# Kernel tuning notes

Hardware: AMD Instinct MI355X
Metric: run time of the kernel (lower is better)

## Reference

```python
import jax, jax.numpy as jnp
import numpy as np

B, S, F_, D, H, L, OUT = 2, 1024, 240, 512, 6, 6, 512
NH = 16
DH = D // NH
EPS = 1e-6  # fast_transformers causal-linear eps
LN_EPS = 1e-5  # torch LayerNorm default


def layernorm(x, g, b):
    m = x.mean(-1, keepdims=True)
    v = ((x - m) ** 2).mean(-1, keepdims=True)
    return (x - m) * jax.lax.rsqrt(v + LN_EPS) * g + b


def causal_linear_attn(q, k, v):
    # q,k,v: [B,S,NH,DH]; feature map phi(x)=elu(x)+1 (fast_transformers default)
    Q = jax.nn.elu(q) + 1.0
    K = jax.nn.elu(k) + 1.0
    # running sum of outer products K_i V_i^T -> [B,S,NH,DH,DH]
    kv = jnp.cumsum(jnp.einsum('bshd,bshm->bshdm', K, v), axis=1)
    num = jnp.einsum('bshd,bshdm->bshm', Q, kv)
    Z = 1.0 / (jnp.einsum('bshd,bshd->bsh', Q, jnp.cumsum(K, axis=1)) + EPS)
    return num * Z[..., None]


def setup_inputs() -> dict:
    key = jax.random.key(0)
    ks = iter(jax.random.split(key, 16))

    def w(shape, s=0.02):
        return (s * jax.random.normal(next(ks), shape)).astype(jnp.float32)

    f32 = jnp.float32
    return {
        'x': jax.random.normal(next(ks), (B, S, F_), dtype=f32),
        'g_in': jnp.ones((F_,), f32), 'b_in': jnp.zeros((F_,), f32),
        'W_pre': w((F_, D)), 'b_pre': jnp.zeros((D,), f32),
        'Wq': w((L, D, D)), 'bq': jnp.zeros((L, D), f32),
        'Wk': w((L, D, D)), 'bk': jnp.zeros((L, D), f32),
        'Wv': w((L, D, D)), 'bv': jnp.zeros((L, D), f32),
        'Wo': w((L, D, D)), 'bo': jnp.zeros((L, D), f32),
        'W1': w((L, D, D)), 'bf1': jnp.zeros((L, D), f32),  # feed_forward_dimensions == hidden_sz
        'W2': w((L, D, D)), 'bf2': jnp.zeros((L, D), f32),
        'ln1_g': jnp.ones((L, D), f32), 'ln1_b': jnp.zeros((L, D), f32),
        'ln2_g': jnp.ones((L, D), f32), 'ln2_b': jnp.zeros((L, D), f32),
        'lnf_g': jnp.ones((D,), f32), 'lnf_b': jnp.zeros((D,), f32),
        'W_post': w((D, OUT)), 'b_post': jnp.zeros((OUT,), f32),
    }


def reference(x, g_in, b_in, W_pre, b_pre, Wq, bq, Wk, bk, Wv, bv, Wo, bo,
              W1, bf1, W2, bf2, ln1_g, ln1_b, ln2_g, ln2_b, lnf_g, lnf_b,
              W_post, b_post):
    # input norm + pre projection
    h = layernorm(x, g_in, b_in) @ W_pre + b_pre  # [B,S,D]
    # fast_transformers post-norm encoder layers
    for l in range(L):
        q = (h @ Wq[l] + bq[l]).reshape(B, S, NH, DH)
        k = (h @ Wk[l] + bk[l]).reshape(B, S, NH, DH)
        v = (h @ Wv[l] + bv[l]).reshape(B, S, NH, DH)
        a = causal_linear_attn(q, k, v).reshape(B, S, D) @ Wo[l] + bo[l]
        h = layernorm(h + a, ln1_g[l], ln1_b[l])
        y = jax.nn.relu(h @ W1[l] + bf1[l]) @ W2[l] + bf2[l]
        h = layernorm(h + y, ln2_g[l], ln2_b[l])
    # final encoder norm, then post projection
    h = layernorm(h, lnf_g, lnf_b)
    return h @ W_post + b_post
```

## Files before the change

kernel.cpp:

```cpp
#include <hip/hip_runtime.h>
#include <hip/hip_bf16.h>
#include <cmath>

#define NROW 2048
#define DMODEL 512
#define FIN 240
#define FINPAD 256
#define NHEAD 16
#define DHEAD 32
#define CHUNK 64
#define NCHUNK 16
#define NLAYER 6
#define SEQ 1024
#define QKVLD 1536

typedef __attribute__((ext_vector_type(8))) short bf16x8;
typedef __attribute__((ext_vector_type(4))) float f32x4;
typedef __attribute__((ext_vector_type(4))) unsigned short u16x4;

#define MFMA_BF16 __builtin_amdgcn_mfma_f32_16x16x32_bf16

__device__ __forceinline__ float phi(float x) {
    return x > 0.f ? x + 1.f : expf(x);
}

__device__ __forceinline__ float bf2f(unsigned short u) {
    return __uint_as_float((unsigned)u << 16);
}

__device__ __forceinline__ unsigned short f2bf_bits(float z) {
    __hip_bfloat16 hb_ = __float2bfloat16(z);
    return *reinterpret_cast<unsigned short*>(&hb_);
}

__device__ __forceinline__ void load_lds16(const void* g, void* l) {
    __builtin_amdgcn_global_load_lds(
        (const __attribute__((address_space(1))) void*)g,
        (__attribute__((address_space(3))) void*)l, 16, 0, 0);
}

__global__ __launch_bounds__(64) void ln_kernel(
    const float* __restrict__ in, const float* __restrict__ res,
    const float* __restrict__ g, const float* __restrict__ b,
    float* __restrict__ out, __hip_bfloat16* __restrict__ outb,
    int C, int Cpad) {
    int row = blockIdx.x;
    int t = threadIdx.x;
    const float* xr = in + (size_t)row * C;
    const float* rr = res ? res + (size_t)row * C : nullptr;
    f32x4 v[2] = {{0.f,0.f,0.f,0.f},{0.f,0.f,0.f,0.f}};
    float sum = 0.f, sq = 0.f;
#pragma unroll
    for (int i = 0; i < 2; ++i) {
        int c = (t + i * 64) * 4;
        if (c < C) {
            f32x4 x_ = *(const f32x4*)&xr[c];
            if (rr) x_ += *(const f32x4*)&rr[c];
            v[i] = x_;
#pragma unroll
            for (int j = 0; j < 4; ++j) { sum += x_[j]; sq += x_[j] * x_[j]; }
        }
    }
#pragma unroll
    for (int off = 32; off > 0; off >>= 1) {
        sum += __shfl_xor(sum, off, 64);
        sq  += __shfl_xor(sq,  off, 64);
    }
    float mean = sum / (float)C;
    float var  = sq / (float)C - mean * mean;
    float rstd = rsqrtf(var + 1e-5f);
#pragma unroll
    for (int i = 0; i < 2; ++i) {
        int c = (t + i * 64) * 4;
        f32x4 y;
#pragma unroll
        for (int j = 0; j < 4; ++j) y[j] = (v[i][j] - mean) * rstd;
        if (c < C) {
            f32x4 gg = *(const f32x4*)&g[c];
            f32x4 bb = *(const f32x4*)&b[c];
#pragma unroll
            for (int j = 0; j < 4; ++j) y[j] = y[j] * gg[j] + bb[j];
            if (out) *(f32x4*)&out[(size_t)row * C + c] = y;
        }
        if (outb && c < Cpad) {
            u16x4 o;
#pragma unroll
            for (int j = 0; j < 4; ++j) {
                float z = (c + j < C) ? y[j] : 0.f;
                o[j] = f2bf_bits(z);
            }
            *(u16x4*)&outb[(size_t)row * Cpad + c] = o;
        }
    }
}

template<int RELU, int WF32, int WBF16, int PHI, int RES, int K>
__global__ __launch_bounds__(256) void gemm_bf16_kernel(
    const __hip_bfloat16* __restrict__ A, const __hip_bfloat16* __restrict__ Bt,
    const float* __restrict__ bias,
    float* __restrict__ C, __hip_bfloat16* __restrict__ Cb,
    const float* __restrict__ Rres, int N) {
    constexpr int NSTEP = K / 64;
    __shared__ __align__(16) __hip_bfloat16 As[4][64][64];
    __shared__ __align__(16) __hip_bfloat16 Bs[4][64][64];
    const int tid = threadIdx.x, lane = tid & 63, w = tid >> 6;
    const int nN = N >> 6;
    const int bm = (blockIdx.x / nN) * 64;
    const int bn = (blockIdx.x % nN) * 64;

    const int srow  = lane >> 3;
    const int sslot = (lane & 7) ^ srow;
    const size_t aoff = (size_t)srow * K + (size_t)sslot * 8;
    const __hip_bfloat16* gA0 = A  + (size_t)(bm + w * 8) * K + aoff;
    const __hip_bfloat16* gA1 = A  + (size_t)(bm + 32 + w * 8) * K + aoff;
    const __hip_bfloat16* gB0 = Bt + (size_t)(bn + w * 8) * K + aoff;
    const __hip_bfloat16* gB1 = Bt + (size_t)(bn + 32 + w * 8) * K + aoff;

#define STAGE(t) do { \
        load_lds16(gA0 + (size_t)(t) * 64, &As[(t) & 3][w * 8][0]); \
        load_lds16(gA1 + (size_t)(t) * 64, &As[(t) & 3][32 + w * 8][0]); \
        load_lds16(gB0 + (size_t)(t) * 64, &Bs[(t) & 3][w * 8][0]); \
        load_lds16(gB1 + (size_t)(t) * 64, &Bs[(t) & 3][32 + w * 8][0]); \
    } while (0)

    const int wm = (w >> 1) << 5, wn = (w & 1) << 5;
    const int fr = lane & 15, fq = lane >> 4;
    const int sw = fr & 7;
    const int e0 = ((fq      ^ sw) << 3);
    const int e1 = (((fq | 4) ^ sw) << 3);
    f32x4 acc00 = {0.f, 0.f, 0.f, 0.f}, acc01 = acc00, acc10 = acc00, acc11 = acc00;

    STAGE(0); STAGE(1); STAGE(2);
#pragma unroll
    for (int t = 0; t < NSTEP; ++t) {
        if (NSTEP - t >= 3)      asm volatile("s_waitcnt vmcnt(8)" ::: "memory");
        else if (NSTEP - t == 2) asm volatile("s_waitcnt vmcnt(4)" ::: "memory");
        else                     asm volatile("s_waitcnt vmcnt(0)" ::: "memory");
        __builtin_amdgcn_s_barrier();
        __builtin_amdgcn_sched_barrier(0);
        if (t + 3 < NSTEP) STAGE(t + 3);
        const int b = t & 3;
        bf16x8 a00 = *(const bf16x8*)&As[b][wm + fr][e0];
        bf16x8 a01 = *(const bf16x8*)&As[b][wm + fr][e1];
        bf16x8 a10 = *(const bf16x8*)&As[b][wm + 16 + fr][e0];
        bf16x8 a11 = *(const bf16x8*)&As[b][wm + 16 + fr][e1];
        bf16x8 b00 = *(const bf16x8*)&Bs[b][wn + fr][e0];
        bf16x8 b01 = *(const bf16x8*)&Bs[b][wn + fr][e1];
        bf16x8 b10 = *(const bf16x8*)&Bs[b][wn + 16 + fr][e0];
        bf16x8 b11 = *(const bf16x8*)&Bs[b][wn + 16 + fr][e1];
        acc00 = MFMA_BF16(a00, b00, acc00, 0, 0, 0);
        acc01 = MFMA_BF16(a00, b10, acc01, 0, 0, 0);
        acc10 = MFMA_BF16(a10, b00, acc10, 0, 0, 0);
        acc11 = MFMA_BF16(a10, b10, acc11, 0, 0, 0);
        acc00 = MFMA_BF16(a01, b01, acc00, 0, 0, 0);
        acc01 = MFMA_BF16(a01, b11, acc01, 0, 0, 0);
        acc10 = MFMA_BF16(a11, b01, acc10, 0, 0, 0);
        acc11 = MFMA_BF16(a11, b11, acc11, 0, 0, 0);
    }
#undef STAGE

    const int orow = bm + wm + (fq << 2);
    const int ocol = bn + wn + fr;
    float bv0 = bias[ocol], bv1 = bias[ocol + 16];
    f32x4 accs[2][2] = {{acc00, acc01}, {acc10, acc11}};
#pragma unroll
    for (int i = 0; i < 2; ++i)
#pragma unroll
        for (int r = 0; r < 4; ++r) {
            int row = orow + i * 16 + r;
            float v0 = accs[i][0][r] + bv0;
            float v1 = accs[i][1][r] + bv1;
            if (RES) {
                v0 += Rres[(size_t)row * N + ocol];
                v1 += Rres[(size_t)row * N + ocol + 16];
            }
            if (RELU) { v0 = fmaxf(v0, 0.f); v1 = fmaxf(v1, 0.f); }
            if (PHI) {
                if (ocol < 1024)      v0 = phi(v0);
                if (ocol + 16 < 1024) v1 = phi(v1);
            }
            if (WF32) {
                C[(size_t)row * N + ocol]      = v0;
                C[(size_t)row * N + ocol + 16] = v1;
            }
            if (WBF16) {
                Cb[(size_t)row * N + ocol]      = __float2bfloat16(v0);
                Cb[(size_t)row * N + ocol + 16] = __float2bfloat16(v1);
            }
        }
}

__global__ __launch_bounds__(256) void wconv_kernel(
    const float* __restrict__ W_pre, const float* __restrict__ Wq,
    const float* __restrict__ Wk, const float* __restrict__ Wv,
    const float* __restrict__ Wo, const float* __restrict__ W1,
    const float* __restrict__ W2, const float* __restrict__ W_post,
    const float* __restrict__ bq, const float* __restrict__ bk,
    const float* __restrict__ bv, float* __restrict__ qkvbias,
    __hip_bfloat16* wpre_t, __hip_bfloat16* wqkv_t, __hip_bfloat16* wo_t,
    __hip_bfloat16* w1_t, __hip_bfloat16* w2_t, __hip_bfloat16* wpost_t) {
    __shared__ float tile[64][65];
    int tb = blockIdx.x;
    if (tb >= 2400) {
        int l = tb - 2400;
        for (int i = threadIdx.x; i < 512; i += 256) {
            qkvbias[l * QKVLD + i]        = bq[l * DMODEL + i];
            qkvbias[l * QKVLD + 512 + i]  = bk[l * DMODEL + i];
            qkvbias[l * QKVLD + 1024 + i] = bv[l * DMODEL + i];
        }
        return;
    }
    const float* src; __hip_bfloat16* dst; int K, Kpad, kt, nt;
    if (tb < 32) {
        src = W_pre; dst = wpre_t; K = FIN; Kpad = FINPAD;
        kt = tb >> 3; nt = tb & 7;
    } else {
        int t2 = tb - 32; int mat = t2 >> 6; int tt = t2 & 63;
        kt = tt >> 3; nt = tt & 7; K = 512; Kpad = 512;
        if (mat == 36) { src = W_post; dst = wpost_t; }
        else {
            int l = mat / 6, j = mat % 6;
            const size_t WSZ = 262144;
            switch (j) {
                case 0: src = Wq + l * WSZ; dst = wqkv_t + l * 786432;          break;
                case 1: src = Wk + l * WSZ; dst = wqkv_t + l * 786432 + 262144; break;
                case 2: src = Wv + l * WSZ; dst = wqkv_t + l * 786432 + 524288; break;
                case 3: src = Wo + l * WSZ; dst = wo_t + l * WSZ;               break;
                case 4: src = W1 + l * WSZ; dst = w1_t + l * WSZ;               break;
                default: src = W2 + l * WSZ; dst = w2_t + l * WSZ;              break;
            }
        }
    }
    const int N = 512;
    int t = threadIdx.x;
    int k0 = kt * 64, n0 = nt * 64;
#pragma unroll
    for (int i = 0; i < 16; ++i) {
        int kk = (t >> 6) * 16 + i;
        int nn = t & 63;
        int k = k0 + kk;
        tile[kk][nn] = (k < K) ? src[(size_t)k * N + n0 + nn] : 0.f;
    }
    __syncthreads();
#pragma unroll
    for (int i = 0; i < 16; ++i) {
        int nn = (t >> 6) * 16 + i;
        int kk = t & 63;
        dst[(size_t)(n0 + nn) * Kpad + k0 + kk] = __float2bfloat16(tile[kk][nn]);
    }
}

__global__ __launch_bounds__(64) void tkv_kernel(
    const __hip_bfloat16* __restrict__ qkvb,
    __hip_bfloat16* __restrict__ Ktg, __hip_bfloat16* __restrict__ Vtg,
    float* __restrict__ ksumg) {
    __shared__ __hip_bfloat16 Kt[32][72];
    __shared__ __hip_bfloat16 Vt[32][72];
    int c = blockIdx.x, hh = blockIdx.y, b = blockIdx.z;
    int t = threadIdx.x;
    int sub = t >> 2, slot = t & 3;
    size_t rb = ((size_t)(b * SEQ + c * CHUNK)) * QKVLD + hh * DHEAD;
#pragma unroll
    for (int it = 0; it < 4; ++it) {
        int s = it * 16 + sub;
        bf16x8 kv = *(const bf16x8*)&qkvb[rb + (size_t)s * QKVLD + 512 + slot * 8];
        bf16x8 vv = *(const bf16x8*)&qkvb[rb + (size_t)s * QKVLD + 1024 + slot * 8];
#pragma unroll
        for (int i = 0; i < 8; ++i) {
            Kt[slot * 8 + i][s] = ((const __hip_bfloat16*)&kv)[i];
            Vt[slot * 8 + i][s] = ((const __hip_bfloat16*)&vv)[i];
        }
    }
    __syncthreads();
    size_t cb = (size_t)((b * NHEAD + hh) * NCHUNK + c);
    __hip_bfloat16* ko = Ktg + cb * 2048;
    __hip_bfloat16* vo = Vtg + cb * 2048;
    int d = t >> 1, s0 = (t & 1) * 32;
#pragma unroll
    for (int i = 0; i < 4; ++i) {
        *(bf16x8*)&ko[d * 64 + s0 + i * 8] = *(const bf16x8*)&Kt[d][s0 + i * 8];
        *(bf16x8*)&vo[d * 64 + s0 + i * 8] = *(const bf16x8*)&Vt[d][s0 + i * 8];
    }
    if (t < 32) {
        float s_ = 0.f;
        for (int s = 0; s < CHUNK; ++s) s_ += __bfloat162float(Kt[t][s]);
        ksumg[cb * 32 + t] = s_;
    }
}

__global__ __launch_bounds__(256) void attn_fused_kernel(
    const __hip_bfloat16* __restrict__ qkvb,
    const __hip_bfloat16* __restrict__ Ktg, const __hip_bfloat16* __restrict__ Vtg,
    const float* __restrict__ ksumg,
    __hip_bfloat16* __restrict__ out) {
    __shared__ __hip_bfloat16 Awb[64][72];
    __shared__ __hip_bfloat16 Stb[32][40];
    __shared__ float den[64];
    __shared__ float ksml[32];
    int c = blockIdx.x, hh = blockIdx.y, b = blockIdx.z;
    int tid = threadIdx.x, lane = tid & 63, w = tid >> 6;
    int fr = lane & 15, fq = lane >> 4;
    size_t chb = (size_t)(b * NHEAD + hh) * NCHUNK;

    if (tid < 32) {
        float s_ = 0.f;
        for (int cp = 0; cp < c; ++cp) s_ += ksumg[(chb + cp) * 32 + tid];
        ksml[tid] = s_;
    }
    int wr = w >> 1, wc = w & 1;
    f32x4 sacc = {0.f, 0.f, 0.f, 0.f};
    const __hip_bfloat16* vq = Vtg + chb * 2048 + (size_t)(wr * 16 + fr) * 64 + fq * 8;
    const __hip_bfloat16* kq = Ktg + chb * 2048 + (size_t)(wc * 16 + fr) * 64 + fq * 8;
    for (int cp = 0; cp < c; ++cp) {
        bf16x8 av0 = *(const bf16x8*)(vq + cp * 2048);
        bf16x8 av1 = *(const bf16x8*)(vq + cp * 2048 + 32);
        bf16x8 bk0 = *(const bf16x8*)(kq + cp * 2048);
        bf16x8 bk1 = *(const bf16x8*)(kq + cp * 2048 + 32);
        sacc = MFMA_BF16(av0, bk0, sacc, 0, 0, 0);
        sacc = MFMA_BF16(av1, bk1, sacc, 0, 0, 0);
    }
#pragma unroll
    for (int r = 0; r < 4; ++r)
        Stb[wr * 16 + fq * 4 + r][wc * 16 + fr] = __float2bfloat16(sacc[r]);

    size_t rb = ((size_t)(b * SEQ + c * CHUNK)) * QKVLD + hh * DHEAD;
    bf16x8 aQ = *(const bf16x8*)&qkvb[rb + (size_t)(w * 16 + fr) * QKVLD + fq * 8];
    f32x4 p[4];
#pragma unroll
    for (int j = 0; j < 4; ++j) {
        f32x4 z = {0.f, 0.f, 0.f, 0.f};
        bf16x8 bK = *(const bf16x8*)&qkvb[rb + (size_t)(j * 16 + fr) * QKVLD + 512 + fq * 8];
        p[j] = MFMA_BF16(aQ, bK, z, 0, 0, 0);
    }
    float rs[4] = {0.f, 0.f, 0.f, 0.f};
#pragma unroll
    for (int j = 0; j < 4; ++j) {
        int tcol = j * 16 + fr;
#pragma unroll
        for (int r = 0; r < 4; ++r) {
            int s = w * 16 + fq * 4 + r;
            float val = (tcol <= s) ? p[j][r] : 0.f;
            p[j][r] = val;
            rs[r] += val;
        }
    }
#pragma unroll
    for (int off = 8; off > 0; off >>= 1) {
#pragma unroll
        for (int r = 0; r < 4; ++r) rs[r] += __shfl_xor(rs[r], off, 64);
    }
    if (fr == 0) {
#pragma unroll
        for (int r = 0; r < 4; ++r) den[w * 16 + fq * 4 + r] = rs[r];
    }
#pragma unroll
    for (int j = 0; j < 4; ++j)
#pragma unroll
        for (int r = 0; r < 4; ++r)
            Awb[w * 16 + fq * 4 + r][j * 16 + fr] = __float2bfloat16(p[j][r]);
    __syncthreads();

    float qk = 0.f;
#pragma unroll
    for (int jj = 0; jj < 8; ++jj)
        qk += __bfloat162float(((const __hip_bfloat16*)&aQ)[jj]) * ksml[fq * 8 + jj];
    qk += __shfl_xor(qk, 16, 64);
    qk += __shfl_xor(qk, 32, 64);
    if (fq == 0)
        den[w * 16 + fr] = 1.f / (den[w * 16 + fr] + qk + 1e-6f);

    size_t orb = ((size_t)(b * SEQ + c * CHUNK)) * DMODEL + hh * DHEAD;
    const __hip_bfloat16* vc = Vtg + (chb + c) * 2048;
#pragma unroll
    for (int mf = 0; mf < 2; ++mf) {
        f32x4 acc = {0.f, 0.f, 0.f, 0.f};
        bf16x8 bS = *(const bf16x8*)&Stb[mf * 16 + fr][fq * 8];
        acc = MFMA_BF16(aQ, bS, acc, 0, 0, 0);
#pragma unroll
        for (int ks = 0; ks < 2; ++ks) {
            bf16x8 aA = *(const bf16x8*)&Awb[w * 16 + fr][ks * 32 + fq * 8];
            bf16x8 bV = *(const bf16x8*)&vc[(size_t)(mf * 16 + fr) * 64 + ks * 32 + fq * 8];
            acc = MFMA_BF16(aA, bV, acc, 0, 0, 0);
        }
#pragma unroll
        for (int r = 0; r < 4; ++r) {
            int s = w * 16 + fq * 4 + r;
            out[orb + (size_t)s * DMODEL + mf * 16 + fr] =
                __float2bfloat16(acc[r] * den[s]);
        }
    }
}

template<int R, int WF, int WB, int PHI, int RES, int K>
static inline void gemm(const __hip_bfloat16* A, const __hip_bfloat16* Bt,
                        const float* bias, float* C, __hip_bfloat16* Cb,
                        const float* Rres, int M, int N, hipStream_t s) {
    gemm_bf16_kernel<R, WF, WB, PHI, RES, K>
        <<<(M / 64) * (N / 64), 256, 0, s>>>(A, Bt, bias, C, Cb, Rres, N);
}

extern "C" void kernel_launch(void* const* d_in, const int* in_sizes, int n_in,
                              void* d_out, int out_size, void* d_ws, size_t ws_size,
                              hipStream_t stream) {
    const float* x      = (const float*)d_in[0];
    const float* g_in   = (const float*)d_in[1];
    const float* b_in   = (const float*)d_in[2];
    const float* W_pre  = (const float*)d_in[3];
    const float* b_pre  = (const float*)d_in[4];
    const float* Wq     = (const float*)d_in[5];
    const float* bq     = (const float*)d_in[6];
    const float* Wk     = (const float*)d_in[7];
    const float* bk     = (const float*)d_in[8];
    const float* Wv     = (const float*)d_in[9];
    const float* bv     = (const float*)d_in[10];
    const float* Wo     = (const float*)d_in[11];
    const float* bo     = (const float*)d_in[12];
    const float* W1     = (const float*)d_in[13];
    const float* bf1    = (const float*)d_in[14];
    const float* W2     = (const float*)d_in[15];
    const float* bf2    = (const float*)d_in[16];
    const float* ln1_g  = (const float*)d_in[17];
    const float* ln1_b  = (const float*)d_in[18];
    const float* ln2_g  = (const float*)d_in[19];
    const float* ln2_b  = (const float*)d_in[20];
    const float* lnf_g  = (const float*)d_in[21];
    const float* lnf_b  = (const float*)d_in[22];
    const float* W_post = (const float*)d_in[23];
    const float* b_post = (const float*)d_in[24];
    (void)in_sizes; (void)n_in; (void)out_size; (void)ws_size;

    float* ws = (float*)d_ws;
    const size_t SZ = (size_t)NROW * DMODEL;
    float* h       = ws;
    float* t1      = h + SZ;
    float* ksumg   = t1 + SZ;
    float* qkvbias = ksumg + 16384;
    __hip_bfloat16* bp = (__hip_bfloat16*)(qkvbias + 9216);
    __hip_bfloat16* Ktg    = bp;            bp += 1048576;
    __hip_bfloat16* Vtg    = bp;            bp += 1048576;
    __hip_bfloat16* hb     = bp;            bp += SZ;
    __hip_bfloat16* qkvb   = bp;            bp += (size_t)NROW * QKVLD;
    __hip_bfloat16* xnb    = bp;            bp += (size_t)NROW * FINPAD;
    __hip_bfloat16* attb   = bp;            bp += SZ;
    __hip_bfloat16* ffb    = bp;            bp += SZ;
    __hip_bfloat16* t0b    = bp;            bp += SZ;
    __hip_bfloat16* wpre_t = bp;            bp += (size_t)DMODEL * FINPAD;
    __hip_bfloat16* wqkv_t = bp;            bp += (size_t)NLAYER * 786432;
    __hip_bfloat16* wo_t   = bp;            bp += (size_t)NLAYER * 262144;
    __hip_bfloat16* w1_t   = bp;            bp += (size_t)NLAYER * 262144;
    __hip_bfloat16* w2_t   = bp;            bp += (size_t)NLAYER * 262144;
    __hip_bfloat16* wpost_t= bp;

    wconv_kernel<<<2406, 256, 0, stream>>>(
        W_pre, Wq, Wk, Wv, Wo, W1, W2, W_post,
        bq, bk, bv, qkvbias,
        wpre_t, wqkv_t, wo_t, w1_t, w2_t, wpost_t);

    ln_kernel<<<NROW, 64, 0, stream>>>(x, nullptr, g_in, b_in, nullptr, xnb, FIN, FINPAD);
    gemm<0, 1, 1, 0, 0, FINPAD>(xnb, wpre_t, b_pre, h, hb, nullptr, NROW, DMODEL, stream);

    dim3 ag(NCHUNK, NHEAD, 2);
    for (int l = 0; l < NLAYER; ++l) {
        gemm<0, 0, 1, 1, 0, DMODEL>(hb, wqkv_t + (size_t)l * 786432, qkvbias + l * QKVLD,
                                    nullptr, qkvb, nullptr, NROW, QKVLD, stream);
        tkv_kernel<<<ag, 64, 0, stream>>>(qkvb, Ktg, Vtg, ksumg);
        attn_fused_kernel<<<ag, 256, 0, stream>>>(qkvb, Ktg, Vtg, ksumg, attb);
        gemm<0, 1, 0, 0, 1, DMODEL>(attb, wo_t + (size_t)l * 262144, bo + l * DMODEL,
                                    t1, nullptr, h, NROW, DMODEL, stream);
        ln_kernel<<<NROW, 64, 0, stream>>>(t1, nullptr, ln1_g + l * DMODEL, ln1_b + l * DMODEL,
                                           h, hb, DMODEL, DMODEL);
        gemm<1, 0, 1, 0, 0, DMODEL>(hb, w1_t + (size_t)l * 262144, bf1 + l * DMODEL,
                                    nullptr, ffb, nullptr, NROW, DMODEL, stream);
        gemm<0, 1, 0, 0, 1, DMODEL>(ffb, w2_t + (size_t)l * 262144, bf2 + l * DMODEL,
                                    t1, nullptr, h, NROW, DMODEL, stream);
        ln_kernel<<<NROW, 64, 0, stream>>>(t1, nullptr, ln2_g + l * DMODEL, ln2_b + l * DMODEL,
                                           h, hb, DMODEL, DMODEL);
    }

    ln_kernel<<<NROW, 64, 0, stream>>>(h, nullptr, lnf_g, lnf_b, nullptr, t0b, DMODEL, DMODEL);
    gemm<0, 1, 0, 0, 0, DMODEL>(t0b, wpost_t, b_post, (float*)d_out, nullptr, nullptr, NROW, DMODEL, stream);
}
```

Measured before the change: 407.6 us.

## Fuse K/V transpose and attention into one sequential-chunk attention kernel

Measured after the change: 383.7 us. -5.9%, faster.

```diff
diff --git a/kernel.cpp b/kernel.cpp
--- a/kernel.cpp
+++ b/kernel.cpp
@@ -13,6 +13,8 @@
 #define NLAYER 6
 #define SEQ 1024
 #define QKVLD 1536
+#define QSPLIT 8
+#define CPQ (NCHUNK / QSPLIT)
 
 typedef __attribute__((ext_vector_type(8))) short bf16x8;
 typedef __attribute__((ext_vector_type(4))) float f32x4;
@@ -22,10 +24,6 @@
 
 __device__ __forceinline__ float phi(float x) {
     return x > 0.f ? x + 1.f : expf(x);
-}
-
-__device__ __forceinline__ float bf2f(unsigned short u) {
-    return __uint_as_float((unsigned)u << 16);
 }
 
 __device__ __forceinline__ unsigned short f2bf_bits(float z) {
@@ -40,14 +38,13 @@
 }
 
 __global__ __launch_bounds__(64) void ln_kernel(
-    const float* __restrict__ in, const float* __restrict__ res,
+    const float* __restrict__ in,
     const float* __restrict__ g, const float* __restrict__ b,
     float* __restrict__ out, __hip_bfloat16* __restrict__ outb,
     int C, int Cpad) {
     int row = blockIdx.x;
     int t = threadIdx.x;
     const float* xr = in + (size_t)row * C;
-    const float* rr = res ? res + (size_t)row * C : nullptr;
     f32x4 v[2] = {{0.f,0.f,0.f,0.f},{0.f,0.f,0.f,0.f}};
     float sum = 0.f, sq = 0.f;
 #pragma unroll
@@ -55,7 +52,6 @@
         int c = (t + i * 64) * 4;
         if (c < C) {
             f32x4 x_ = *(const f32x4*)&xr[c];
-            if (rr) x_ += *(const f32x4*)&rr[c];
             v[i] = x_;
 #pragma unroll
             for (int j = 0; j < 4; ++j) { sum += x_[j]; sq += x_[j] * x_[j]; }
@@ -250,144 +246,128 @@
     }
 }
 
-__global__ __launch_bounds__(64) void tkv_kernel(
+__global__ __launch_bounds__(256) void attn_seq_kernel(
     const __hip_bfloat16* __restrict__ qkvb,
-    __hip_bfloat16* __restrict__ Ktg, __hip_bfloat16* __restrict__ Vtg,
-    float* __restrict__ ksumg) {
+    __hip_bfloat16* __restrict__ out) {
     __shared__ __hip_bfloat16 Kt[32][72];
     __shared__ __hip_bfloat16 Vt[32][72];
-    int c = blockIdx.x, hh = blockIdx.y, b = blockIdx.z;
-    int t = threadIdx.x;
-    int sub = t >> 2, slot = t & 3;
-    size_t rb = ((size_t)(b * SEQ + c * CHUNK)) * QKVLD + hh * DHEAD;
-#pragma unroll
-    for (int it = 0; it < 4; ++it) {
-        int s = it * 16 + sub;
-        bf16x8 kv = *(const bf16x8*)&qkvb[rb + (size_t)s * QKVLD + 512 + slot * 8];
-        bf16x8 vv = *(const bf16x8*)&qkvb[rb + (size_t)s * QKVLD + 1024 + slot * 8];
-#pragma unroll
-        for (int i = 0; i < 8; ++i) {
-            Kt[slot * 8 + i][s] = ((const __hip_bfloat16*)&kv)[i];
-            Vt[slot * 8 + i][s] = ((const __hip_bfloat16*)&vv)[i];
-        }
-    }
-    __syncthreads();
-    size_t cb = (size_t)((b * NHEAD + hh) * NCHUNK + c);
-    __hip_bfloat16* ko = Ktg + cb * 2048;
-    __hip_bfloat16* vo = Vtg + cb * 2048;
-    int d = t >> 1, s0 = (t & 1) * 32;
-#pragma unroll
-    for (int i = 0; i < 4; ++i) {
-        *(bf16x8*)&ko[d * 64 + s0 + i * 8] = *(const bf16x8*)&Kt[d][s0 + i * 8];
-        *(bf16x8*)&vo[d * 64 + s0 + i * 8] = *(const bf16x8*)&Vt[d][s0 + i * 8];
-    }
-    if (t < 32) {
-        float s_ = 0.f;
-        for (int s = 0; s < CHUNK; ++s) s_ += __bfloat162float(Kt[t][s]);
-        ksumg[cb * 32 + t] = s_;
-    }
-}
-
-__global__ __launch_bounds__(256) void attn_fused_kernel(
-    const __hip_bfloat16* __restrict__ qkvb,
-    const __hip_bfloat16* __restrict__ Ktg, const __hip_bfloat16* __restrict__ Vtg,
-    const float* __restrict__ ksumg,
-    __hip_bfloat16* __restrict__ out) {
+    __shared__ __hip_bfloat16 Qs[64][40];
+    __shared__ __hip_bfloat16 Ks[64][40];
     __shared__ __hip_bfloat16 Awb[64][72];
     __shared__ __hip_bfloat16 Stb[32][40];
     __shared__ float den[64];
     __shared__ float ksml[32];
-    int c = blockIdx.x, hh = blockIdx.y, b = blockIdx.z;
+    int q = blockIdx.x, hh = blockIdx.y, b = blockIdx.z;
     int tid = threadIdx.x, lane = tid & 63, w = tid >> 6;
     int fr = lane & 15, fq = lane >> 4;
-    size_t chb = (size_t)(b * NHEAD + hh) * NCHUNK;
-
-    if (tid < 32) {
-        float s_ = 0.f;
-        for (int cp = 0; cp < c; ++cp) s_ += ksumg[(chb + cp) * 32 + tid];
-        ksml[tid] = s_;
-    }
     int wr = w >> 1, wc = w & 1;
+    int srow = tid >> 2, slot = tid & 3;
+    if (tid < 32) ksml[tid] = 0.f;
     f32x4 sacc = {0.f, 0.f, 0.f, 0.f};
-    const __hip_bfloat16* vq = Vtg + chb * 2048 + (size_t)(wr * 16 + fr) * 64 + fq * 8;
-    const __hip_bfloat16* kq = Ktg + chb * 2048 + (size_t)(wc * 16 + fr) * 64 + fq * 8;
-    for (int cp = 0; cp < c; ++cp) {
-        bf16x8 av0 = *(const bf16x8*)(vq + cp * 2048);
-        bf16x8 av1 = *(const bf16x8*)(vq + cp * 2048 + 32);
-        bf16x8 bk0 = *(const bf16x8*)(kq + cp * 2048);
-        bf16x8 bk1 = *(const bf16x8*)(kq + cp * 2048 + 32);
-        sacc = MFMA_BF16(av0, bk0, sacc, 0, 0, 0);
-        sacc = MFMA_BF16(av1, bk1, sacc, 0, 0, 0);
-    }
-#pragma unroll
-    for (int r = 0; r < 4; ++r)
-        Stb[wr * 16 + fq * 4 + r][wc * 16 + fr] = __float2bfloat16(sacc[r]);
-
-    size_t rb = ((size_t)(b * SEQ + c * CHUNK)) * QKVLD + hh * DHEAD;
-    bf16x8 aQ = *(const bf16x8*)&qkvb[rb + (size_t)(w * 16 + fr) * QKVLD + fq * 8];
-    f32x4 p[4];
-#pragma unroll
-    for (int j = 0; j < 4; ++j) {
-        f32x4 z = {0.f, 0.f, 0.f, 0.f};
-        bf16x8 bK = *(const bf16x8*)&qkvb[rb + (size_t)(j * 16 + fr) * QKVLD + 512 + fq * 8];
-        p[j] = MFMA_BF16(aQ, bK, z, 0, 0, 0);
-    }
-    float rs[4] = {0.f, 0.f, 0.f, 0.f};
-#pragma unroll
-    for (int j = 0; j < 4; ++j) {
-        int tcol = j * 16 + fr;
-#pragma unroll
-        for (int r = 0; r < 4; ++r) {
-            int s = w * 16 + fq * 4 + r;
-            float val = (tcol <= s) ? p[j][r] : 0.f;
-            p[j][r] = val;
-            rs[r] += val;
-        }
-    }
-#pragma unroll
-    for (int off = 8; off > 0; off >>= 1) {
-#pragma unroll
-        for (int r = 0; r < 4; ++r) rs[r] += __shfl_xor(rs[r], off, 64);
-    }
-    if (fr == 0) {
-#pragma unroll
-        for (int r = 0; r < 4; ++r) den[w * 16 + fq * 4 + r] = rs[r];
-    }
-#pragma unroll
-    for (int j = 0; j < 4; ++j)
-#pragma unroll
-        for (int r = 0; r < 4; ++r)
-            Awb[w * 16 + fq * 4 + r][j * 16 + fr] = __float2bfloat16(p[j][r]);
+    const int cstart = q * CPQ, cend = cstart + CPQ;
     __syncthreads();
-
-    float qk = 0.f;
-#pragma unroll
-    for (int jj = 0; jj < 8; ++jj)
-        qk += __bfloat162float(((const __hip_bfloat16*)&aQ)[jj]) * ksml[fq * 8 + jj];
-    qk += __shfl_xor(qk, 16, 64);
-    qk += __shfl_xor(qk, 32, 64);
-    if (fq == 0)
-        den[w * 16 + fr] = 1.f / (den[w * 16 + fr] + qk + 1e-6f);
-
-    size_t orb = ((size_t)(b * SEQ + c * CHUNK)) * DMODEL + hh * DHEAD;
-    const __hip_bfloat16* vc = Vtg + (chb + c) * 2048;
-#pragma unroll
-    for (int mf = 0; mf < 2; ++mf) {
-        f32x4 acc = {0.f, 0.f, 0.f, 0.f};
-        bf16x8 bS = *(const bf16x8*)&Stb[mf * 16 + fr][fq * 8];
-        acc = MFMA_BF16(aQ, bS, acc, 0, 0, 0);
-#pragma unroll
-        for (int ks = 0; ks < 2; ++ks) {
-            bf16x8 aA = *(const bf16x8*)&Awb[w * 16 + fr][ks * 32 + fq * 8];
-            bf16x8 bV = *(const bf16x8*)&vc[(size_t)(mf * 16 + fr) * 64 + ks * 32 + fq * 8];
-            acc = MFMA_BF16(aA, bV, acc, 0, 0, 0);
-        }
-#pragma unroll
-        for (int r = 0; r < 4; ++r) {
-            int s = w * 16 + fq * 4 + r;
-            out[orb + (size_t)s * DMODEL + mf * 16 + fr] =
-                __float2bfloat16(acc[r] * den[s]);
-        }
+    for (int cp = 0; cp < cend; ++cp) {
+        const bool owned = cp >= cstart;
+        size_t rb = ((size_t)(b * SEQ + cp * CHUNK)) * QKVLD + hh * DHEAD;
+        bf16x8 kv = *(const bf16x8*)&qkvb[rb + (size_t)srow * QKVLD + 512 + slot * 8];
+        bf16x8 vv = *(const bf16x8*)&qkvb[rb + (size_t)srow * QKVLD + 1024 + slot * 8];
+#pragma unroll
+        for (int i = 0; i < 8; ++i) {
+            Kt[slot * 8 + i][srow] = ((const __hip_bfloat16*)&kv)[i];
+            Vt[slot * 8 + i][srow] = ((const __hip_bfloat16*)&vv)[i];
+        }
+        if (owned) {
+            *(bf16x8*)&Qs[srow][slot * 8] =
+                *(const bf16x8*)&qkvb[rb + (size_t)srow * QKVLD + slot * 8];
+            *(bf16x8*)&Ks[srow][slot * 8] = kv;
+#pragma unroll
+            for (int r = 0; r < 4; ++r)
+                Stb[wr * 16 + fq * 4 + r][wc * 16 + fr] = __float2bfloat16(sacc[r]);
+        }
+        __syncthreads();
+        if (owned) {
+            bf16x8 aQ = *(const bf16x8*)&Qs[w * 16 + fr][fq * 8];
+            f32x4 p[4];
+#pragma unroll
+            for (int j = 0; j < 4; ++j) {
+                f32x4 z = {0.f, 0.f, 0.f, 0.f};
+                bf16x8 bK = *(const bf16x8*)&Ks[j * 16 + fr][fq * 8];
+                p[j] = MFMA_BF16(aQ, bK, z, 0, 0, 0);
+            }
+            float rs[4] = {0.f, 0.f, 0.f, 0.f};
+#pragma unroll
+            for (int j = 0; j < 4; ++j) {
+                int tcol = j * 16 + fr;
+#pragma unroll
+                for (int r = 0; r < 4; ++r) {
+                    int s = w * 16 + fq * 4 + r;
+                    float val = (tcol <= s) ? p[j][r] : 0.f;
+                    p[j][r] = val;
+                    rs[r] += val;
+                }
+            }
+#pragma unroll
+            for (int off = 8; off > 0; off >>= 1) {
+#pragma unroll
+                for (int r = 0; r < 4; ++r) rs[r] += __shfl_xor(rs[r], off, 64);
+            }
+            if (fr == 0) {
+#pragma unroll
+                for (int r = 0; r < 4; ++r) den[w * 16 + fq * 4 + r] = rs[r];
+            }
+#pragma unroll
+            for (int j = 0; j < 4; ++j)
+#pragma unroll
+                for (int r = 0; r < 4; ++r)
+                    Awb[w * 16 + fq * 4 + r][j * 16 + fr] = __float2bfloat16(p[j][r]);
+            __syncthreads();
+            float qk = 0.f;
+#pragma unroll
+            for (int jj = 0; jj < 8; ++jj)
+                qk += __bfloat162float(((const __hip_bfloat16*)&aQ)[jj]) * ksml[fq * 8 + jj];
+            qk += __shfl_xor(qk, 16, 64);
+            qk += __shfl_xor(qk, 32, 64);
+            if (fq == 0)
+                den[w * 16 + fr] = 1.f / (den[w * 16 + fr] + qk + 1e-6f);
+            __syncthreads();
+            size_t orb = ((size_t)(b * SEQ + cp * CHUNK)) * DMODEL + hh * DHEAD;
+#pragma unroll
+            for (int mf = 0; mf < 2; ++mf) {
+                f32x4 acc = {0.f, 0.f, 0.f, 0.f};
+                bf16x8 bS = *(const bf16x8*)&Stb[mf * 16 + fr][fq * 8];
+                acc = MFMA_BF16(aQ, bS, acc, 0, 0, 0);
+#pragma unroll
+                for (int ks = 0; ks < 2; ++ks) {
+                    bf16x8 aA = *(const bf16x8*)&Awb[w * 16 + fr][ks * 32 + fq * 8];
+                    bf16x8 bV = *(const bf16x8*)&Vt[mf * 16 + fr][ks * 32 + fq * 8];
+                    acc = MFMA_BF16(aA, bV, acc, 0, 0, 0);
+                }
+#pragma unroll
+                for (int r = 0; r < 4; ++r) {
+                    int s = w * 16 + fq * 4 + r;
+                    out[orb + (size_t)s * DMODEL + mf * 16 + fr] =
+                        __float2bfloat16(acc[r] * den[s]);
+                }
+            }
+        }
+        if (cp + 1 < cend) {
+            bf16x8 v0 = *(const bf16x8*)&Vt[wr * 16 + fr][fq * 8];
+            bf16x8 v1 = *(const bf16x8*)&Vt[wr * 16 + fr][32 + fq * 8];
+            bf16x8 k0 = *(const bf16x8*)&Kt[wc * 16 + fr][fq * 8];
+            bf16x8 k1 = *(const bf16x8*)&Kt[wc * 16 + fr][32 + fq * 8];
+            sacc = MFMA_BF16(v0, k0, sacc, 0, 0, 0);
+            sacc = MFMA_BF16(v1, k1, sacc, 0, 0, 0);
+            int d = tid >> 3, s0 = (tid & 7) * 8;
+            float part = 0.f;
+#pragma unroll
+            for (int i = 0; i < 8; ++i)
+                part += __bfloat162float(Kt[d][s0 + i]);
+            part += __shfl_xor(part, 1, 64);
+            part += __shfl_xor(part, 2, 64);
+            part += __shfl_xor(part, 4, 64);
+            if ((tid & 7) == 0) ksml[d] += part;
+        }
+        __syncthreads();
     }
 }
 
@@ -433,11 +413,8 @@
     const size_t SZ = (size_t)NROW * DMODEL;
     float* h       = ws;
     float* t1      = h + SZ;
-    float* ksumg   = t1 + SZ;
-    float* qkvbias = ksumg + 16384;
+    float* qkvbias = t1 + SZ;
     __hip_bfloat16* bp = (__hip_bfloat16*)(qkvbias + 9216);
-    __hip_bfloat16* Ktg    = bp;            bp += 1048576;
-    __hip_bfloat16* Vtg    = bp;            bp += 1048576;
     __hip_bfloat16* hb     = bp;            bp += SZ;
     __hip_bfloat16* qkvb   = bp;            bp += (size_t)NROW * QKVLD;
     __hip_bfloat16* xnb    = bp;            bp += (size_t)NROW * FINPAD;
@@ -456,27 +433,26 @@
         bq, bk, bv, qkvbias,
         wpre_t, wqkv_t, wo_t, w1_t, w2_t, wpost_t);
 
-    ln_kernel<<<NROW, 64, 0, stream>>>(x, nullptr, g_in, b_in, nullptr, xnb, FIN, FINPAD);
+    ln_kernel<<<NROW, 64, 0, stream>>>(x, g_in, b_in, nullptr, xnb, FIN, FINPAD);
     gemm<0, 1, 1, 0, 0, FINPAD>(xnb, wpre_t, b_pre, h, hb, nullptr, NROW, DMODEL, stream);
 
-    dim3 ag(NCHUNK, NHEAD, 2);
+    dim3 ag(QSPLIT, NHEAD, 2);
     for (int l = 0; l < NLAYER; ++l) {
         gemm<0, 0, 1, 1, 0, DMODEL>(hb, wqkv_t + (size_t)l * 786432, qkvbias + l * QKVLD,
                                     nullptr, qkvb, nullptr, NROW, QKVLD, stream);
-        tkv_kernel<<<ag, 64, 0, stream>>>(qkvb, Ktg, Vtg, ksumg);
-        attn_fused_kernel<<<ag, 256, 0, stream>>>(qkvb, Ktg, Vtg, ksumg, attb);
+        attn_seq_kernel<<<ag, 256, 0, stream>>>(qkvb, attb);
         gemm<0, 1, 0, 0, 1, DMODEL>(attb, wo_t + (size_t)l * 262144, bo + l * DMODEL,
                                     t1, nullptr, h, NROW, DMODEL, stream);
-        ln_kernel<<<NROW, 64, 0, stream>>>(t1, nullptr, ln1_g + l * DMODEL, ln1_b + l * DMODEL,
+        ln_kernel<<<NROW, 64, 0, stream>>>(t1, ln1_g + l * DMODEL, ln1_b + l * DMODEL,
                                            h, hb, DMODEL, DMODEL);
         gemm<1, 0, 1, 0, 0, DMODEL>(hb, w1_t + (size_t)l * 262144, bf1 + l * DMODEL,
                                     nullptr, ffb, nullptr, NROW, DMODEL, stream);
         gemm<0, 1, 0, 0, 1, DMODEL>(ffb, w2_t + (size_t)l * 262144, bf2 + l * DMODEL,
                                     t1, nullptr, h, NROW, DMODEL, stream);
-        ln_kernel<<<NROW, 64, 0, stream>>>(t1, nullptr, ln2_g + l * DMODEL, ln2_b + l * DMODEL,
+        ln_kernel<<<NROW, 64, 0, stream>>>(t1, ln2_g + l * DMODEL, ln2_b + l * DMODEL,
                                            h, hb, DMODEL, DMODEL);
     }
 
-    ln_kernel<<<NROW, 64, 0, stream>>>(h, nullptr, lnf_g, lnf_b, nullptr, t0b, DMODEL, DMODEL);
+    ln_kernel<<<NROW, 64, 0, stream>>>(h, lnf_g, lnf_b, nullptr, t0b, DMODEL, DMODEL);
     gemm<0, 1, 0, 0, 0, DMODEL>(t0b, wpost_t, b_post, (float*)d_out, nullptr, nullptr, NROW, DMODEL, stream);
 }
```
